# Kernel tuning notes

Hardware: AMD Instinct MI355X
Metric: run time of the kernel (lower is better)

Reference implementation:

```python
import jax, jax.numpy as jnp
import numpy as np

H = 128

def _gru_cell(x, h, w_ih, w_hh, b_ih, b_hh):
    # PyTorch GRUCell semantics; w_* are [3H, H], gate order r, z, n.
    gi = x @ w_ih.T + b_ih
    gh = h @ w_hh.T + b_hh
    ir, iz, in_ = jnp.split(gi, 3, axis=-1)
    hr, hz, hn = jnp.split(gh, 3, axis=-1)
    r = jax.nn.sigmoid(ir + hr)
    z = jax.nn.sigmoid(iz + hz)
    n = jnp.tanh(in_ + r * hn)
    return (1.0 - z) * n + z * h


def setup_inputs() -> dict:
    key = jax.random.key(0)
    ks = jax.random.split(key, 24)
    s = 0.05
    d = {}
    d["weapon_features"] = jax.random.normal(ks[0], (4, 8, 64, 4), jnp.float32)
    d["target_features"] = jax.random.normal(ks[1], (4, 8, 64, 4), jnp.float32)
    d["edge_features"] = jax.random.uniform(ks[2], (4, 8, 64, 64, 1), jnp.float32)
    # projections (torch Linear convention: weight [out, in])
    d["wp_w"] = jax.random.normal(ks[3], (H, 4), jnp.float32) * s
    d["wp_b"] = jnp.zeros((H,), jnp.float32)
    d["tp_w"] = jax.random.normal(ks[4], (H, 4), jnp.float32) * s
    d["tp_b"] = jnp.zeros((H,), jnp.float32)
    d["ep_w"] = jax.random.normal(ks[5], (H, 1), jnp.float32) * s
    d["ep_b"] = jnp.zeros((H,), jnp.float32)
    # message / edge-update linears [H, 3H]
    d["eu_w"] = jax.random.normal(ks[6], (H, 3 * H), jnp.float32) * s
    d["eu_b"] = jnp.zeros((H,), jnp.float32)
    d["wm_w"] = jax.random.normal(ks[7], (H, 3 * H), jnp.float32) * s
    d["wm_b"] = jnp.zeros((H,), jnp.float32)
    d["tm_w"] = jax.random.normal(ks[8], (H, 3 * H), jnp.float32) * s
    d["tm_b"] = jnp.zeros((H,), jnp.float32)
    # GRU cells
    d["gru_w_ih_w"] = jax.random.normal(ks[9], (3 * H, H), jnp.float32) * s
    d["gru_w_hh_w"] = jax.random.normal(ks[10], (3 * H, H), jnp.float32) * s
    d["gru_b_ih_w"] = jnp.zeros((3 * H,), jnp.float32)
    d["gru_b_hh_w"] = jnp.zeros((3 * H,), jnp.float32)
    d["gru_w_ih_t"] = jax.random.normal(ks[11], (3 * H, H), jnp.float32) * s
    d["gru_w_hh_t"] = jax.random.normal(ks[12], (3 * H, H), jnp.float32) * s
    d["gru_b_ih_t"] = jnp.zeros((3 * H,), jnp.float32)
    d["gru_b_hh_t"] = jnp.zeros((3 * H,), jnp.float32)
    return d


def reference(weapon_features, target_features, edge_features,
              wp_w, wp_b, tp_w, tp_b, ep_w, ep_b,
              eu_w, eu_b, wm_w, wm_b, tm_w, tm_b,
              gru_w_ih_w, gru_w_hh_w, gru_b_ih_w, gru_b_hh_w,
              gru_w_ih_t, gru_w_hh_t, gru_b_ih_t, gru_b_hh_t):
    B, P, W = weapon_features.shape[:3]
    T = target_features.shape[2]
    h = wp_w.shape[0]

    weapon_h = weapon_features @ wp_w.T + wp_b          # [B,P,W,H]
    target_h = target_features @ tp_w.T + tp_b          # [B,P,T,H]
    edge_h = edge_features @ ep_w.T + ep_b              # [B,P,W,T,H]

    # edge_update(cat([w_exp, t_exp, edge_h])) == sum of three slice-linears,
    # broadcast-added; avoids materializing the [B,P,W,T,3H] concat.
    ea, eb, ec = eu_w[:, :h], eu_w[:, h:2 * h], eu_w[:, 2 * h:]
    edge_pre = ((weapon_h @ ea.T)[:, :, :, None, :]
                + (target_h @ eb.T)[:, :, None, :, :]
                + edge_h @ ec.T + eu_b)
    edge_h_new = jnp.tanh(edge_pre)                     # [B,P,W,T,H]

    # weapon_msg(cat([w_exp, t_exp, edge_h_new])).sum(dim=3)
    wa, wb, wc = wm_w[:, :h], wm_w[:, h:2 * h], wm_w[:, 2 * h:]
    weapon_msgs = (T * (weapon_h @ wa.T)
                   + (target_h.sum(axis=2) @ wb.T)[:, :, None, :]
                   + edge_h_new.sum(axis=3) @ wc.T
                   + T * wm_b)                          # [B,P,W,H]

    # target_msg(cat([t_exp, w_exp, edge_h_new])).sum(dim=2)
    ta, tb, tc = tm_w[:, :h], tm_w[:, h:2 * h], tm_w[:, 2 * h:]
    target_msgs = (W * (target_h @ ta.T)
                   + (weapon_h.sum(axis=2) @ tb.T)[:, :, None, :]
                   + edge_h_new.sum(axis=2) @ tc.T
                   + W * tm_b)                          # [B,P,T,H]

    weapon_h_new = _gru_cell(weapon_msgs.reshape(-1, h), weapon_h.reshape(-1, h),
                             gru_w_ih_w, gru_w_hh_w, gru_b_ih_w, gru_b_hh_w)
    weapon_h_new = weapon_h_new.reshape(B, P, W, h)

    target_h_new = _gru_cell(target_msgs.reshape(-1, h), target_h.reshape(-1, h),
                             gru_w_ih_t, gru_w_hh_t, gru_b_ih_t, gru_b_hh_t)
    target_h_new = target_h_new.reshape(B, P, T, h)

    return weapon_h_new, target_h_new, edge_h_new
```

## Files before the change

### kernel.cpp

```cpp
#include <hip/hip_runtime.h>

#define DEV __device__ __forceinline__

constexpr int H  = 128;
constexpr int BP = 32;
constexpr int NR = 2048;

constexpr int WH_OFF    = 0;
constexpr int TH_OFF    = WH_OFF + NR*H;
constexpr int WHS_OFF   = TH_OFF + NR*H;
constexpr int THS_OFF   = WHS_OFF + BP*H;
constexpr int V1_OFF    = THS_OFF + BP*H;
constexpr int C0_OFF    = V1_OFF + H;
constexpr int WT1_OFF   = C0_OFF + H;
constexpr int WT2_OFF   = WT1_OFF + 128*640;
constexpr int WCT_OFF   = WT2_OFF + 128*640;
constexpr int TCT_OFF   = WCT_OFF + 128*128;
constexpr int WIHWT_OFF = TCT_OFF + 128*128;
constexpr int WIHTT_OFF = WIHWT_OFF + 128*384;
constexpr int WBT_OFF   = WIHTT_OFF + 128*384;
constexpr int TBT_OFF   = WBT_OFF + 128*128;
constexpr int OUT1_OFF  = TBT_OFF + 128*128;
constexpr int OUT2_OFF  = OUT1_OFF + NR*640;
constexpr int ESW_OFF   = OUT2_OFF + NR*640;
constexpr int ESTP_OFF  = ESW_OFF + NR*H;
constexpr int MSGW_OFF  = ESTP_OFF + 16*NR*H;
constexpr int MSGT_OFF  = MSGW_OFF + NR*H;
constexpr int GIW_OFF   = MSGT_OFF + NR*H;
constexpr int GIT_OFF   = GIW_OFF + NR*384;
constexpr int WBV_OFF   = GIT_OFF + NR*384;
constexpr int TBV_OFF   = WBV_OFF + BP*H;

DEV float fast_tanh(float x) {
  float e = __builtin_amdgcn_exp2f(x * 2.8853900817779268f);
  return fmaf(-2.0f, __builtin_amdgcn_rcpf(e + 1.0f), 1.0f);
}
DEV float fast_sigmoid(float x) {
  float e = __builtin_amdgcn_exp2f(x * -1.4426950408889634f);
  return __builtin_amdgcn_rcpf(1.0f + e);
}

__global__ __launch_bounds__(256) void k0_transpose(
    const float* __restrict__ eu_w, const float* __restrict__ wm_w,
    const float* __restrict__ tm_w,
    const float* __restrict__ whh_w, const float* __restrict__ whh_t,
    const float* __restrict__ wih_w, const float* __restrict__ wih_t,
    float* __restrict__ ws)
{
  __shared__ float T[128*133];
  int tt = blockIdx.x, tid = threadIdx.x;
  const float* src; int rs = 384, co = 0, row0 = 0, dsto, ldd, j0;
  switch (tt) {
    case 0:  src=eu_w;  dsto=WT1_OFF; ldd=640; j0=0;   break;
    case 1:  src=wm_w;  dsto=WT1_OFF; ldd=640; j0=128; break;
    case 2: case 3: case 4:
      src=whh_w; rs=128; row0=(tt-2)*128; dsto=WT1_OFF; ldd=640; j0=256+(tt-2)*128; break;
    case 5:  src=eu_w;  co=128; dsto=WT2_OFF; ldd=640; j0=0; break;
    case 6:  src=tm_w;  dsto=WT2_OFF; ldd=640; j0=128; break;
    case 7: case 8: case 9:
      src=whh_t; rs=128; row0=(tt-7)*128; dsto=WT2_OFF; ldd=640; j0=256+(tt-7)*128; break;
    case 10: src=wm_w; co=256; dsto=WCT_OFF; ldd=128; j0=0; break;
    case 11: src=tm_w; co=256; dsto=TCT_OFF; ldd=128; j0=0; break;
    case 12: src=wm_w; co=128; dsto=WBT_OFF; ldd=128; j0=0; break;
    case 13: src=tm_w; co=128; dsto=TBT_OFF; ldd=128; j0=0; break;
    case 14: case 15: case 16:
      src=wih_w; rs=128; row0=(tt-14)*128; dsto=WIHWT_OFF; ldd=384; j0=(tt-14)*128; break;
    default:
      src=wih_t; rs=128; row0=(tt-17)*128; dsto=WIHTT_OFF; ldd=384; j0=(tt-17)*128; break;
  }
  #pragma unroll
  for (int q = 0; q < 16; ++q) {
    int idx = q*1024 + tid*4;
    int r = idx >> 7, c = idx & 127;
    float4 v = *(const float4*)&src[(row0 + r)*rs + co + c];
    float* t = &T[r*133 + c];
    t[0]=v.x; t[1]=v.y; t[2]=v.z; t[3]=v.w;
  }
  __syncthreads();
  float* dst = ws + dsto;
  #pragma unroll
  for (int q = 0; q < 64; ++q) {
    int idx = q*256 + tid;
    int k = idx >> 7, j = idx & 127;
    dst[k*ldd + j0 + j] = T[j*133 + k];
  }
}

__global__ __launch_bounds__(256) void k1_proj(
    const float* __restrict__ wf, const float* __restrict__ tf,
    const float* __restrict__ wp_w, const float* __restrict__ wp_b,
    const float* __restrict__ tp_w, const float* __restrict__ tp_b,
    const float* __restrict__ eu_w,
    const float* __restrict__ ep_w, const float* __restrict__ ep_b,
    const float* __restrict__ eu_b,
    float* __restrict__ ws)
{
  __shared__ float fs[2][32][4];
  int bid = blockIdx.x, tid = threadIdx.x;
  if (bid < 2048) {
    int gid = bid*256 + tid;
    int m = gid >> 7;
    int j = gid & 127;
    int side = m >> 11;
    int n = m & 2047;
    const float* F  = side ? tf : wf;
    const float* Pw = side ? tp_w : wp_w;
    const float* Pb = side ? tp_b : wp_b;
    float4 x  = *(const float4*)&F[n*4];
    float4 wv = *(const float4*)&Pw[j*4];
    float v = x.x*wv.x + x.y*wv.y + x.z*wv.z + x.w*wv.w + Pb[j];
    ws[(side ? TH_OFF : WH_OFF) + n*H + j] = v;
  } else {
    {
      int side = tid >> 7, r = tid & 127;
      int bp = r >> 2, c = r & 3;
      const float* F = side ? tf : wf;
      float s = 0.f;
      #pragma unroll 8
      for (int w = 0; w < 64; ++w) s += F[bp*256 + w*4 + c];
      fs[side][bp][c] = s;
    }
    __syncthreads();
    {
      int side = tid >> 7, j = tid & 127;
      const float* Pw = side ? tp_w : wp_w;
      const float* Pb = side ? tp_b : wp_b;
      float4 wv = *(const float4*)&Pw[j*4];
      float pb = Pb[j] * 64.f;
      float* dst = ws + (side ? THS_OFF : WHS_OFF) + j;
      #pragma unroll 4
      for (int bp = 0; bp < 32; ++bp) {
        float4 f = *(const float4*)&fs[side][bp][0];
        dst[bp*128] = f.x*wv.x + f.y*wv.y + f.z*wv.z + f.w*wv.w + pb;
      }
    }
    if (tid < 128) {
      int j = tid;
      float s1 = 0.f, s0 = 0.f;
      for (int k = 0; k < 128; ++k) {
        float ec = eu_w[j*384 + 256 + k];
        s1 = fmaf(ec, ep_w[k], s1);
        s0 = fmaf(ec, ep_b[k], s0);
      }
      ws[V1_OFF + j] = s1;
      ws[C0_OFF + j] = s0 + eu_b[j];
    }
  }
}

#define FMA4(A, s, Wv) do { A.x = fmaf(s, Wv.x, A.x); A.y = fmaf(s, Wv.y, A.y); \
                            A.z = fmaf(s, Wv.z, A.z); A.w = fmaf(s, Wv.w, A.w); } while (0)

DEV void stage_x_direct(float* Xs, const float* __restrict__ X, int row0, int tid) {
  const float* src = X + row0*128;
  #pragma unroll
  for (int q = 0; q < 4; ++q) {
    int idx = q*1024 + tid*4;
    *(float4*)&Xs[idx] = *(const float4*)&src[idx];
  }
}

DEV void stage_x_sum16(float* Xs, const float* __restrict__ base, int row0, int tid) {
  #pragma unroll
  for (int q = 0; q < 4; ++q) {
    int idx = q*1024 + tid*4;
    float4 s = *(const float4*)&base[row0*128 + idx];
    #pragma unroll
    for (int wt = 1; wt < 16; ++wt) {
      float4 v = *(const float4*)&base[wt*(NR*H) + row0*128 + idx];
      s.x += v.x; s.y += v.y; s.z += v.z; s.w += v.w;
    }
    *(float4*)&Xs[idx] = s;
  }
}

DEV void gemm_core(const float* __restrict__ Wt, int ldw, int j0,
                   const float* Xs, float* Ws, int tid, float4 acc[4])
{
  const int tc = tid & 31, tr = tid >> 5;
  const int jj = tc*4, r0 = tr*4;
  #pragma unroll
  for (int i = 0; i < 4; ++i) acc[i] = make_float4(0.f, 0.f, 0.f, 0.f);
  for (int kc = 0; kc < 128; kc += 32) {
    __syncthreads();
    #pragma unroll
    for (int q = 0; q < 4; ++q) {
      int idx = q*1024 + tid*4;
      int kk = idx >> 7, j = idx & 127;
      *(float4*)&Ws[idx] = *(const float4*)&Wt[(kc+kk)*ldw + j0 + j];
    }
    __syncthreads();
    #pragma unroll
    for (int kk = 0; kk < 32; kk += 4) {
      float4 w0 = *(const float4*)&Ws[(kk+0)*128 + jj];
      float4 w1 = *(const float4*)&Ws[(kk+1)*128 + jj];
      float4 w2 = *(const float4*)&Ws[(kk+2)*128 + jj];
      float4 w3 = *(const float4*)&Ws[(kk+3)*128 + jj];
      #pragma unroll
      for (int rr = 0; rr < 4; ++rr) {
        float4 xq = *(const float4*)&Xs[(r0+rr)*128 + kc + kk];
        FMA4(acc[rr], xq.x, w0);
        FMA4(acc[rr], xq.y, w1);
        FMA4(acc[rr], xq.z, w2);
        FMA4(acc[rr], xq.w, w3);
      }
    }
  }
}

__global__ __launch_bounds__(256) void k3_gemm1(float* __restrict__ ws)
{
  __shared__ float Xs[32*128];
  __shared__ float Wsh[32*128];
  int bid = blockIdx.x, tid = threadIdx.x;
  const int tc = tid & 31, tr = tid >> 5;
  const int jj = tc*4, r0 = tr*4;
  float4 acc[4];
  if (bid < 640) {
    int side = bid >= 320;
    int b2 = bid - (side ? 320 : 0);
    int rt = b2 & 63, ct = b2 >> 6;
    int row0 = rt*32;
    stage_x_direct(Xs, ws + (side ? TH_OFF : WH_OFF), row0, tid);
    gemm_core(ws + (side ? WT2_OFF : WT1_OFF), 640, ct*128, Xs, Wsh, tid, acc);
    float* C = ws + (side ? OUT2_OFF : OUT1_OFF);
    #pragma unroll
    for (int rr = 0; rr < 4; ++rr)
      *(float4*)&C[(row0+r0+rr)*640 + ct*128 + jj] = acc[rr];
  } else {
    int which = bid - 640;
    stage_x_direct(Xs, ws + (which ? WHS_OFF : THS_OFF), 0, tid);
    gemm_core(ws + (which ? TBT_OFF : WBT_OFF), 128, 0, Xs, Wsh, tid, acc);
    float* C = ws + (which ? TBV_OFF : WBV_OFF);
    #pragma unroll
    for (int rr = 0; rr < 4; ++rr)
      *(float4*)&C[(r0+rr)*128 + jj] = acc[rr];
  }
}

__global__ __launch_bounds__(256) void k4_edge(
    const float* __restrict__ ef, float* __restrict__ ws, float* __restrict__ out)
{
  __shared__ float Bs[64*128];
  __shared__ float e_lds[4*64];
  __shared__ float red[2][4][128];
  int bid = blockIdx.x, tid = threadIdx.x;
  int bp = bid >> 4, wq = bid & 15;
  int j = tid & 127, tsel = tid >> 7;
  float v1j = ws[V1_OFF + j], c0j = ws[C0_OFF + j];
  {
    const float* o2 = ws + OUT2_OFF + bp*64*640;
    #pragma unroll
    for (int q = 0; q < 8; ++q) {
      int idx = q*256 + tid;
      int t = idx >> 5, jq = (idx & 31)*4;
      *(float4*)&Bs[t*128 + jq] = *(const float4*)&o2[t*640 + jq];
    }
  }
  if (tid < 64) {
    int w = tid >> 4, t4 = (tid & 15)*4;
    *(float4*)&e_lds[w*64 + t4] = *(const float4*)&ef[bp*4096 + (wq*4 + w)*64 + t4];
  }
  float a_reg[4];
  #pragma unroll
  for (int w = 0; w < 4; ++w)
    a_reg[w] = ws[OUT1_OFF + (bp*64 + wq*4 + w)*640 + j];
  __syncthreads();
  float tsum[4] = {0.f, 0.f, 0.f, 0.f};
  float* edst = out + 524288 + (bp*64 + wq*4)*8192 + j;
  float* pdst = ws + ESTP_OFF + wq*(NR*H) + bp*64*128 + j;
  for (int i = 0; i < 32; ++i) {
    int t = 2*i + tsel;
    float base = Bs[t*128 + j] + c0j;
    float wsum = 0.f;
    #pragma unroll
    for (int w = 0; w < 4; ++w) {
      float ev = e_lds[w*64 + t];
      float pre = a_reg[w] + fmaf(ev, v1j, base);
      float hv = fast_tanh(pre);
      __builtin_nontemporal_store(hv, &edst[w*8192 + t*128]);
      tsum[w] += hv;
      wsum += hv;
    }
    pdst[t*128] = wsum;
  }
  #pragma unroll
  for (int w = 0; w < 4; ++w) red[tsel][w][j] = tsum[w];
  __syncthreads();
  if (tsel == 0) {
    #pragma unroll
    for (int w = 0; w < 4; ++w)
      ws[ESW_OFF + (bp*64 + wq*4 + w)*128 + j] = red[0][w][j] + red[1][w][j];
  }
}

__global__ __launch_bounds__(256) void k5_gemm2(
    float* __restrict__ ws, const float* __restrict__ wm_b, const float* __restrict__ tm_b)
{
  __shared__ float Xs[32*128];
  __shared__ float Wsh[32*128];
  int bid = blockIdx.x, tid = threadIdx.x;
  int side = bid >> 6, rt = bid & 63;
  int row0 = rt*32;
  const int tc = tid & 31, tr = tid >> 5;
  const int jj = tc*4, r0 = tr*4;
  if (side == 0) stage_x_direct(Xs, ws + ESW_OFF, row0, tid);
  else           stage_x_sum16(Xs, ws + ESTP_OFF, row0, tid);
  float4 acc[4];
  gemm_core(ws + (side ? TCT_OFF : WCT_OFF), 128, 0, Xs, Wsh, tid, acc);
  const float* OUTx = ws + (side ? OUT2_OFF : OUT1_OFF);
  const float* BV   = ws + (side ? TBV_OFF : WBV_OFF);
  const float* mb   = side ? tm_b : wm_b;
  float* MSG        = ws + (side ? MSGT_OFF : MSGW_OFF);
  float4 b4 = *(const float4*)&mb[jj];
  #pragma unroll
  for (int rr = 0; rr < 4; ++rr) {
    int n = row0 + r0 + rr;
    float4 wa4 = *(const float4*)&OUTx[n*640 + 128 + jj];
    float4 bv4 = *(const float4*)&BV[(n >> 6)*128 + jj];
    float4 r;
    r.x = acc[rr].x + 64.f*(wa4.x + b4.x) + bv4.x;
    r.y = acc[rr].y + 64.f*(wa4.y + b4.y) + bv4.y;
    r.z = acc[rr].z + 64.f*(wa4.z + b4.z) + bv4.z;
    r.w = acc[rr].w + 64.f*(wa4.w + b4.w) + bv4.w;
    *(float4*)&MSG[n*128 + jj] = r;
  }
}

__global__ __launch_bounds__(256) void k6_gemm3(float* __restrict__ ws)
{
  __shared__ float Xs[32*128];
  __shared__ float Wsh[32*128];
  int bid = blockIdx.x, tid = threadIdx.x;
  int side = bid >= 192;
  int b2 = bid - (side ? 192 : 0);
  int rt = b2 & 63, ct = b2 >> 6;
  int row0 = rt*32;
  const int tc = tid & 31, tr = tid >> 5;
  const int jj = tc*4, r0 = tr*4;
  stage_x_direct(Xs, ws + (side ? MSGT_OFF : MSGW_OFF), row0, tid);
  float4 acc[4];
  gemm_core(ws + (side ? WIHTT_OFF : WIHWT_OFF), 384, ct*128, Xs, Wsh, tid, acc);
  float* C = ws + (side ? GIT_OFF : GIW_OFF);
  #pragma unroll
  for (int rr = 0; rr < 4; ++rr)
    *(float4*)&C[(row0+r0+rr)*384 + ct*128 + jj] = acc[rr];
}

__global__ __launch_bounds__(256) void k7_gru(
    const float* __restrict__ ws, float* __restrict__ out,
    const float* __restrict__ bih_w, const float* __restrict__ bhh_w,
    const float* __restrict__ bih_t, const float* __restrict__ bhh_t)
{
  int gid = blockIdx.x*256 + threadIdx.x;
  int m = gid >> 7, j = gid & 127;
  int side = m >> 11, n = m & 2047;
  const float* GI = ws + (side ? GIT_OFF : GIW_OFF) + n*384;
  const float* GH = ws + (side ? OUT2_OFF : OUT1_OFF) + n*640 + 256;
  const float* Hv = ws + (side ? TH_OFF : WH_OFF) + n*128;
  const float* bi = side ? bih_t : bih_w;
  const float* bh = side ? bhh_t : bhh_w;
  float gir = GI[j]       + bi[j];
  float giz = GI[128 + j] + bi[128 + j];
  float gin = GI[256 + j] + bi[256 + j];
  float ghr = GH[j]       + bh[j];
  float ghz = GH[128 + j] + bh[128 + j];
  float ghn = GH[256 + j] + bh[256 + j];
  float r  = fast_sigmoid(gir + ghr);
  float z  = fast_sigmoid(giz + ghz);
  float nn = fast_tanh(gin + r*ghn);
  float h  = Hv[j];
  out[side*262144 + n*128 + j] = (1.f - z)*nn + z*h;
}

extern "C" void kernel_launch(void* const* d_in, const int* in_sizes, int n_in,
                              void* d_out, int out_size, void* d_ws, size_t ws_size,
                              hipStream_t stream)
{
  const float* wf    = (const float*)d_in[0];
  const float* tf    = (const float*)d_in[1];
  const float* ef    = (const float*)d_in[2];
  const float* wp_w  = (const float*)d_in[3];
  const float* wp_b  = (const float*)d_in[4];
  const float* tp_w  = (const float*)d_in[5];
  const float* tp_b  = (const float*)d_in[6];
  const float* ep_w  = (const float*)d_in[7];
  const float* ep_b  = (const float*)d_in[8];
  const float* eu_w  = (const float*)d_in[9];
  const float* eu_b  = (const float*)d_in[10];
  const float* wm_w  = (const float*)d_in[11];
  const float* wm_b  = (const float*)d_in[12];
  const float* tm_w  = (const float*)d_in[13];
  const float* tm_b  = (const float*)d_in[14];
  const float* wih_w = (const float*)d_in[15];
  const float* whh_w = (const float*)d_in[16];
  const float* bih_w = (const float*)d_in[17];
  const float* bhh_w = (const float*)d_in[18];
  const float* wih_t = (const float*)d_in[19];
  const float* whh_t = (const float*)d_in[20];
  const float* bih_t = (const float*)d_in[21];
  const float* bhh_t = (const float*)d_in[22];
  float* ws  = (float*)d_ws;
  float* out = (float*)d_out;

  hipLaunchKernelGGL(k0_transpose, dim3(20), dim3(256), 0, stream,
                     eu_w, wm_w, tm_w, whh_w, whh_t, wih_w, wih_t, ws);
  hipLaunchKernelGGL(k1_proj, dim3(2049), dim3(256), 0, stream,
                     wf, tf, wp_w, wp_b, tp_w, tp_b, eu_w, ep_w, ep_b, eu_b, ws);
  hipLaunchKernelGGL(k3_gemm1, dim3(642),  dim3(256), 0, stream, ws);
  hipLaunchKernelGGL(k4_edge,  dim3(512),  dim3(256), 0, stream, ef, ws, out);
  hipLaunchKernelGGL(k5_gemm2, dim3(128),  dim3(256), 0, stream, ws, wm_b, tm_b);
  hipLaunchKernelGGL(k6_gemm3, dim3(384),  dim3(256), 0, stream, ws);
  hipLaunchKernelGGL(k7_gru,   dim3(2048), dim3(256), 0, stream, ws, out,
                     bih_w, bhh_w, bih_t, bhh_t);
}
```

Before: 189.2 us.

## Merge transpose into projection kernel, enlarge gemm1 tiles, widen edge and GRU work

The weight-transpose kernel becomes extra blocks of the projection kernel, removing one launch. gemm1 moves to 64-row tiles with 8 accumulators per thread to improve weight reuse. The edge kernel now handles 8 weapons per block, which halves the partial target-sum buffers that gemm2 must reduce. The GRU kernel uses float4 loads and nontemporal stores. Each change trades fewer blocks and launches for more registers and LDS per block, which can lower occupancy.

```diff
diff --git a/kernel.cpp b/kernel.cpp
--- a/kernel.cpp
+++ b/kernel.cpp
@@ -24,7 +24,7 @@
 constexpr int OUT2_OFF  = OUT1_OFF + NR*640;
 constexpr int ESW_OFF   = OUT2_OFF + NR*640;
 constexpr int ESTP_OFF  = ESW_OFF + NR*H;
-constexpr int MSGW_OFF  = ESTP_OFF + 16*NR*H;
+constexpr int MSGW_OFF  = ESTP_OFF + 8*NR*H;
 constexpr int MSGT_OFF  = MSGW_OFF + NR*H;
 constexpr int GIW_OFF   = MSGT_OFF + NR*H;
 constexpr int GIT_OFF   = GIW_OFF + NR*384;
@@ -40,62 +40,18 @@
   return __builtin_amdgcn_rcpf(1.0f + e);
 }
 
-__global__ __launch_bounds__(256) void k0_transpose(
+__global__ __launch_bounds__(256) void ka_prep(
+    const float* __restrict__ wf, const float* __restrict__ tf,
+    const float* __restrict__ wp_w, const float* __restrict__ wp_b,
+    const float* __restrict__ tp_w, const float* __restrict__ tp_b,
     const float* __restrict__ eu_w, const float* __restrict__ wm_w,
     const float* __restrict__ tm_w,
     const float* __restrict__ whh_w, const float* __restrict__ whh_t,
     const float* __restrict__ wih_w, const float* __restrict__ wih_t,
-    float* __restrict__ ws)
-{
-  __shared__ float T[128*133];
-  int tt = blockIdx.x, tid = threadIdx.x;
-  const float* src; int rs = 384, co = 0, row0 = 0, dsto, ldd, j0;
-  switch (tt) {
-    case 0:  src=eu_w;  dsto=WT1_OFF; ldd=640; j0=0;   break;
-    case 1:  src=wm_w;  dsto=WT1_OFF; ldd=640; j0=128; break;
-    case 2: case 3: case 4:
-      src=whh_w; rs=128; row0=(tt-2)*128; dsto=WT1_OFF; ldd=640; j0=256+(tt-2)*128; break;
-    case 5:  src=eu_w;  co=128; dsto=WT2_OFF; ldd=640; j0=0; break;
-    case 6:  src=tm_w;  dsto=WT2_OFF; ldd=640; j0=128; break;
-    case 7: case 8: case 9:
-      src=whh_t; rs=128; row0=(tt-7)*128; dsto=WT2_OFF; ldd=640; j0=256+(tt-7)*128; break;
-    case 10: src=wm_w; co=256; dsto=WCT_OFF; ldd=128; j0=0; break;
-    case 11: src=tm_w; co=256; dsto=TCT_OFF; ldd=128; j0=0; break;
-    case 12: src=wm_w; co=128; dsto=WBT_OFF; ldd=128; j0=0; break;
-    case 13: src=tm_w; co=128; dsto=TBT_OFF; ldd=128; j0=0; break;
-    case 14: case 15: case 16:
-      src=wih_w; rs=128; row0=(tt-14)*128; dsto=WIHWT_OFF; ldd=384; j0=(tt-14)*128; break;
-    default:
-      src=wih_t; rs=128; row0=(tt-17)*128; dsto=WIHTT_OFF; ldd=384; j0=(tt-17)*128; break;
-  }
-  #pragma unroll
-  for (int q = 0; q < 16; ++q) {
-    int idx = q*1024 + tid*4;
-    int r = idx >> 7, c = idx & 127;
-    float4 v = *(const float4*)&src[(row0 + r)*rs + co + c];
-    float* t = &T[r*133 + c];
-    t[0]=v.x; t[1]=v.y; t[2]=v.z; t[3]=v.w;
-  }
-  __syncthreads();
-  float* dst = ws + dsto;
-  #pragma unroll
-  for (int q = 0; q < 64; ++q) {
-    int idx = q*256 + tid;
-    int k = idx >> 7, j = idx & 127;
-    dst[k*ldd + j0 + j] = T[j*133 + k];
-  }
-}
-
-__global__ __launch_bounds__(256) void k1_proj(
-    const float* __restrict__ wf, const float* __restrict__ tf,
-    const float* __restrict__ wp_w, const float* __restrict__ wp_b,
-    const float* __restrict__ tp_w, const float* __restrict__ tp_b,
-    const float* __restrict__ eu_w,
     const float* __restrict__ ep_w, const float* __restrict__ ep_b,
     const float* __restrict__ eu_b,
     float* __restrict__ ws)
 {
-  __shared__ float fs[2][32][4];
   int bid = blockIdx.x, tid = threadIdx.x;
   if (bid < 2048) {
     int gid = bid*256 + tid;
@@ -110,7 +66,8 @@
     float4 wv = *(const float4*)&Pw[j*4];
     float v = x.x*wv.x + x.y*wv.y + x.z*wv.z + x.w*wv.w + Pb[j];
     ws[(side ? TH_OFF : WH_OFF) + n*H + j] = v;
-  } else {
+  } else if (bid == 2048) {
+    __shared__ float fs[2][32][4];
     {
       int side = tid >> 7, r = tid & 127;
       int bp = r >> 2, c = r & 3;
@@ -145,13 +102,51 @@
       ws[V1_OFF + j] = s1;
       ws[C0_OFF + j] = s0 + eu_b[j];
     }
+  } else {
+    __shared__ float T[128*133];
+    int tt = bid - 2049;
+    const float* src; int rs = 384, co = 0, row0 = 0, dsto, ldd, j0;
+    switch (tt) {
+      case 0:  src=eu_w;  dsto=WT1_OFF; ldd=640; j0=0;   break;
+      case 1:  src=wm_w;  dsto=WT1_OFF; ldd=640; j0=128; break;
+      case 2: case 3: case 4:
+        src=whh_w; rs=128; row0=(tt-2)*128; dsto=WT1_OFF; ldd=640; j0=256+(tt-2)*128; break;
+      case 5:  src=eu_w;  co=128; dsto=WT2_OFF; ldd=640; j0=0; break;
+      case 6:  src=tm_w;  dsto=WT2_OFF; ldd=640; j0=128; break;
+      case 7: case 8: case 9:
+        src=whh_t; rs=128; row0=(tt-7)*128; dsto=WT2_OFF; ldd=640; j0=256+(tt-7)*128; break;
+      case 10: src=wm_w; co=256; dsto=WCT_OFF; ldd=128; j0=0; break;
+      case 11: src=tm_w; co=256; dsto=TCT_OFF; ldd=128; j0=0; break;
+      case 12: src=wm_w; co=128; dsto=WBT_OFF; ldd=128; j0=0; break;
+      case 13: src=tm_w; co=128; dsto=TBT_OFF; ldd=128; j0=0; break;
+      case 14: case 15: case 16:
+        src=wih_w; rs=128; row0=(tt-14)*128; dsto=WIHWT_OFF; ldd=384; j0=(tt-14)*128; break;
+      default:
+        src=wih_t; rs=128; row0=(tt-17)*128; dsto=WIHTT_OFF; ldd=384; j0=(tt-17)*128; break;
+    }
+    #pragma unroll
+    for (int q = 0; q < 16; ++q) {
+      int idx = q*1024 + tid*4;
+      int r = idx >> 7, c = idx & 127;
+      float4 v = *(const float4*)&src[(row0 + r)*rs + co + c];
+      float* t = &T[r*133 + c];
+      t[0]=v.x; t[1]=v.y; t[2]=v.z; t[3]=v.w;
+    }
+    __syncthreads();
+    float* dst = ws + dsto;
+    #pragma unroll
+    for (int q = 0; q < 64; ++q) {
+      int idx = q*256 + tid;
+      int k = idx >> 7, j = idx & 127;
+      dst[k*ldd + j0 + j] = T[j*133 + k];
+    }
   }
 }
 
 #define FMA4(A, s, Wv) do { A.x = fmaf(s, Wv.x, A.x); A.y = fmaf(s, Wv.y, A.y); \
                             A.z = fmaf(s, Wv.z, A.z); A.w = fmaf(s, Wv.w, A.w); } while (0)
 
-DEV void stage_x_direct(float* Xs, const float* __restrict__ X, int row0, int tid) {
+DEV void stage_x32(float* Xs, const float* __restrict__ X, int row0, int tid) {
   const float* src = X + row0*128;
   #pragma unroll
   for (int q = 0; q < 4; ++q) {
@@ -160,13 +155,22 @@
   }
 }
 
-DEV void stage_x_sum16(float* Xs, const float* __restrict__ base, int row0, int tid) {
+DEV void stage_x64(float* Xs, const float* __restrict__ X, int row0, int tid) {
+  const float* src = X + row0*128;
+  #pragma unroll
+  for (int q = 0; q < 8; ++q) {
+    int idx = q*1024 + tid*4;
+    *(float4*)&Xs[idx] = *(const float4*)&src[idx];
+  }
+}
+
+DEV void stage_x_sum8(float* Xs, const float* __restrict__ base, int row0, int tid) {
   #pragma unroll
   for (int q = 0; q < 4; ++q) {
     int idx = q*1024 + tid*4;
     float4 s = *(const float4*)&base[row0*128 + idx];
     #pragma unroll
-    for (int wt = 1; wt < 16; ++wt) {
+    for (int wt = 1; wt < 8; ++wt) {
       float4 v = *(const float4*)&base[wt*(NR*H) + row0*128 + idx];
       s.x += v.x; s.y += v.y; s.z += v.z; s.w += v.w;
     }
@@ -174,8 +178,8 @@
   }
 }
 
-DEV void gemm_core(const float* __restrict__ Wt, int ldw, int j0,
-                   const float* Xs, float* Ws, int tid, float4 acc[4])
+DEV void gemm_core32(const float* __restrict__ Wt, int ldw, int j0,
+                     const float* Xs, float* Ws, int tid, float4 acc[4])
 {
   const int tc = tid & 31, tr = tid >> 5;
   const int jj = tc*4, r0 = tr*4;
@@ -208,44 +212,81 @@
   }
 }
 
-__global__ __launch_bounds__(256) void k3_gemm1(float* __restrict__ ws)
-{
-  __shared__ float Xs[32*128];
+DEV void gemm_core64(const float* __restrict__ Wt, int ldw, int j0,
+                     const float* Xs, float* Ws, int tid, float4 acc[8])
+{
+  const int tc = tid & 31, tr = tid >> 5;
+  const int jj = tc*4, r0 = tr*8;
+  #pragma unroll
+  for (int i = 0; i < 8; ++i) acc[i] = make_float4(0.f, 0.f, 0.f, 0.f);
+  for (int kc = 0; kc < 128; kc += 32) {
+    __syncthreads();
+    #pragma unroll
+    for (int q = 0; q < 4; ++q) {
+      int idx = q*1024 + tid*4;
+      int kk = idx >> 7, j = idx & 127;
+      *(float4*)&Ws[idx] = *(const float4*)&Wt[(kc+kk)*ldw + j0 + j];
+    }
+    __syncthreads();
+    #pragma unroll
+    for (int kk = 0; kk < 32; kk += 4) {
+      float4 w0 = *(const float4*)&Ws[(kk+0)*128 + jj];
+      float4 w1 = *(const float4*)&Ws[(kk+1)*128 + jj];
+      float4 w2 = *(const float4*)&Ws[(kk+2)*128 + jj];
+      float4 w3 = *(const float4*)&Ws[(kk+3)*128 + jj];
+      #pragma unroll
+      for (int rr = 0; rr < 8; ++rr) {
+        float4 xq = *(const float4*)&Xs[(r0+rr)*128 + kc + kk];
+        FMA4(acc[rr], xq.x, w0);
+        FMA4(acc[rr], xq.y, w1);
+        FMA4(acc[rr], xq.z, w2);
+        FMA4(acc[rr], xq.w, w3);
+      }
+    }
+  }
+}
+
+__global__ __launch_bounds__(256) void kb_gemm1(float* __restrict__ ws)
+{
+  __shared__ float Xs[64*128];
   __shared__ float Wsh[32*128];
   int bid = blockIdx.x, tid = threadIdx.x;
   const int tc = tid & 31, tr = tid >> 5;
-  const int jj = tc*4, r0 = tr*4;
-  float4 acc[4];
-  if (bid < 640) {
-    int side = bid >= 320;
-    int b2 = bid - (side ? 320 : 0);
-    int rt = b2 & 63, ct = b2 >> 6;
-    int row0 = rt*32;
-    stage_x_direct(Xs, ws + (side ? TH_OFF : WH_OFF), row0, tid);
-    gemm_core(ws + (side ? WT2_OFF : WT1_OFF), 640, ct*128, Xs, Wsh, tid, acc);
+  const int jj = tc*4;
+  if (bid < 320) {
+    int side = bid >= 160;
+    int b2 = bid - (side ? 160 : 0);
+    int rt = b2 & 31, ct = b2 >> 5;
+    int row0 = rt*64;
+    stage_x64(Xs, ws + (side ? TH_OFF : WH_OFF), row0, tid);
+    float4 acc[8];
+    gemm_core64(ws + (side ? WT2_OFF : WT1_OFF), 640, ct*128, Xs, Wsh, tid, acc);
     float* C = ws + (side ? OUT2_OFF : OUT1_OFF);
-    #pragma unroll
-    for (int rr = 0; rr < 4; ++rr)
+    const int r0 = tr*8;
+    #pragma unroll
+    for (int rr = 0; rr < 8; ++rr)
       *(float4*)&C[(row0+r0+rr)*640 + ct*128 + jj] = acc[rr];
   } else {
-    int which = bid - 640;
-    stage_x_direct(Xs, ws + (which ? WHS_OFF : THS_OFF), 0, tid);
-    gemm_core(ws + (which ? TBT_OFF : WBT_OFF), 128, 0, Xs, Wsh, tid, acc);
+    int which = bid - 320;
+    stage_x32(Xs, ws + (which ? WHS_OFF : THS_OFF), 0, tid);
+    float4 acc[4];
+    gemm_core32(ws + (which ? TBT_OFF : WBT_OFF), 128, 0, Xs, Wsh, tid, acc);
     float* C = ws + (which ? TBV_OFF : WBV_OFF);
+    const int r0 = tr*4;
     #pragma unroll
     for (int rr = 0; rr < 4; ++rr)
       *(float4*)&C[(r0+rr)*128 + jj] = acc[rr];
   }
 }
 
-__global__ __launch_bounds__(256) void k4_edge(
+__global__ __launch_bounds__(256) void kc_edge(
     const float* __restrict__ ef, float* __restrict__ ws, float* __restrict__ out)
 {
   __shared__ float Bs[64*128];
-  __shared__ float e_lds[4*64];
-  __shared__ float red[2][4][128];
+  __shared__ float e_lds[8*64];
+  __shared__ float red[2][8][128];
   int bid = blockIdx.x, tid = threadIdx.x;
-  int bp = bid >> 4, wq = bid & 15;
+  int bp = bid >> 3, wq = bid & 7;
   int j = tid & 127, tsel = tid >> 7;
   float v1j = ws[V1_OFF + j], c0j = ws[C0_OFF + j];
   {
@@ -257,24 +298,24 @@
       *(float4*)&Bs[t*128 + jq] = *(const float4*)&o2[t*640 + jq];
     }
   }
-  if (tid < 64) {
+  if (tid < 128) {
     int w = tid >> 4, t4 = (tid & 15)*4;
-    *(float4*)&e_lds[w*64 + t4] = *(const float4*)&ef[bp*4096 + (wq*4 + w)*64 + t4];
-  }
-  float a_reg[4];
-  #pragma unroll
-  for (int w = 0; w < 4; ++w)
-    a_reg[w] = ws[OUT1_OFF + (bp*64 + wq*4 + w)*640 + j];
+    *(float4*)&e_lds[w*64 + t4] = *(const float4*)&ef[bp*4096 + (wq*8 + w)*64 + t4];
+  }
+  float a_reg[8];
+  #pragma unroll
+  for (int w = 0; w < 8; ++w)
+    a_reg[w] = ws[OUT1_OFF + (bp*64 + wq*8 + w)*640 + j];
   __syncthreads();
-  float tsum[4] = {0.f, 0.f, 0.f, 0.f};
-  float* edst = out + 524288 + (bp*64 + wq*4)*8192 + j;
+  float tsum[8] = {0,0,0,0,0,0,0,0};
+  float* edst = out + 524288 + (bp*64 + wq*8)*8192 + j;
   float* pdst = ws + ESTP_OFF + wq*(NR*H) + bp*64*128 + j;
   for (int i = 0; i < 32; ++i) {
     int t = 2*i + tsel;
     float base = Bs[t*128 + j] + c0j;
     float wsum = 0.f;
     #pragma unroll
-    for (int w = 0; w < 4; ++w) {
+    for (int w = 0; w < 8; ++w) {
       float ev = e_lds[w*64 + t];
       float pre = a_reg[w] + fmaf(ev, v1j, base);
       float hv = fast_tanh(pre);
@@ -285,16 +326,16 @@
     pdst[t*128] = wsum;
   }
   #pragma unroll
-  for (int w = 0; w < 4; ++w) red[tsel][w][j] = tsum[w];
+  for (int w = 0; w < 8; ++w) red[tsel][w][j] = tsum[w];
   __syncthreads();
   if (tsel == 0) {
     #pragma unroll
-    for (int w = 0; w < 4; ++w)
-      ws[ESW_OFF + (bp*64 + wq*4 + w)*128 + j] = red[0][w][j] + red[1][w][j];
-  }
-}
-
-__global__ __launch_bounds__(256) void k5_gemm2(
+    for (int w = 0; w < 8; ++w)
+      ws[ESW_OFF + (bp*64 + wq*8 + w)*128 + j] = red[0][w][j] + red[1][w][j];
+  }
+}
+
+__global__ __launch_bounds__(256) void kd_gemm2(
     float* __restrict__ ws, const float* __restrict__ wm_b, const float* __restrict__ tm_b)
 {
   __shared__ float Xs[32*128];
@@ -304,10 +345,10 @@
   int row0 = rt*32;
   const int tc = tid & 31, tr = tid >> 5;
   const int jj = tc*4, r0 = tr*4;
-  if (side == 0) stage_x_direct(Xs, ws + ESW_OFF, row0, tid);
-  else           stage_x_sum16(Xs, ws + ESTP_OFF, row0, tid);
+  if (side == 0) stage_x32(Xs, ws + ESW_OFF, row0, tid);
+  else           stage_x_sum8(Xs, ws + ESTP_OFF, row0, tid);
   float4 acc[4];
-  gemm_core(ws + (side ? TCT_OFF : WCT_OFF), 128, 0, Xs, Wsh, tid, acc);
+  gemm_core32(ws + (side ? TCT_OFF : WCT_OFF), 128, 0, Xs, Wsh, tid, acc);
   const float* OUTx = ws + (side ? OUT2_OFF : OUT1_OFF);
   const float* BV   = ws + (side ? TBV_OFF : WBV_OFF);
   const float* mb   = side ? tm_b : wm_b;
@@ -327,7 +368,7 @@
   }
 }
 
-__global__ __launch_bounds__(256) void k6_gemm3(float* __restrict__ ws)
+__global__ __launch_bounds__(256) void ke_gemm3(float* __restrict__ ws)
 {
   __shared__ float Xs[32*128];
   __shared__ float Wsh[32*128];
@@ -338,39 +379,54 @@
   int row0 = rt*32;
   const int tc = tid & 31, tr = tid >> 5;
   const int jj = tc*4, r0 = tr*4;
-  stage_x_direct(Xs, ws + (side ? MSGT_OFF : MSGW_OFF), row0, tid);
+  stage_x32(Xs, ws + (side ? MSGT_OFF : MSGW_OFF), row0, tid);
   float4 acc[4];
-  gemm_core(ws + (side ? WIHTT_OFF : WIHWT_OFF), 384, ct*128, Xs, Wsh, tid, acc);
+  gemm_core32(ws + (side ? WIHTT_OFF : WIHWT_OFF), 384, ct*128, Xs, Wsh, tid, acc);
   float* C = ws + (side ? GIT_OFF : GIW_OFF);
   #pragma unroll
   for (int rr = 0; rr < 4; ++rr)
     *(float4*)&C[(row0+r0+rr)*384 + ct*128 + jj] = acc[rr];
 }
 
-__global__ __launch_bounds__(256) void k7_gru(
+__global__ __launch_bounds__(256) void kf_gru(
     const float* __restrict__ ws, float* __restrict__ out,
     const float* __restrict__ bih_w, const float* __restrict__ bhh_w,
     const float* __restrict__ bih_t, const float* __restrict__ bhh_t)
 {
   int gid = blockIdx.x*256 + threadIdx.x;
-  int m = gid >> 7, j = gid & 127;
-  int side = m >> 11, n = m & 2047;
+  int jj = (gid & 31)*4;
+  int n  = (gid >> 5) & 2047;
+  int side = gid >> 16;
   const float* GI = ws + (side ? GIT_OFF : GIW_OFF) + n*384;
   const float* GH = ws + (side ? OUT2_OFF : OUT1_OFF) + n*640 + 256;
   const float* Hv = ws + (side ? TH_OFF : WH_OFF) + n*128;
   const float* bi = side ? bih_t : bih_w;
   const float* bh = side ? bhh_t : bhh_w;
-  float gir = GI[j]       + bi[j];
-  float giz = GI[128 + j] + bi[128 + j];
-  float gin = GI[256 + j] + bi[256 + j];
-  float ghr = GH[j]       + bh[j];
-  float ghz = GH[128 + j] + bh[128 + j];
-  float ghn = GH[256 + j] + bh[256 + j];
-  float r  = fast_sigmoid(gir + ghr);
-  float z  = fast_sigmoid(giz + ghz);
-  float nn = fast_tanh(gin + r*ghn);
-  float h  = Hv[j];
-  out[side*262144 + n*128 + j] = (1.f - z)*nn + z*h;
+  float4 gir = *(const float4*)&GI[jj];
+  float4 giz = *(const float4*)&GI[128 + jj];
+  float4 gin = *(const float4*)&GI[256 + jj];
+  float4 ghr = *(const float4*)&GH[jj];
+  float4 ghz = *(const float4*)&GH[128 + jj];
+  float4 ghn = *(const float4*)&GH[256 + jj];
+  float4 bir = *(const float4*)&bi[jj];
+  float4 biz = *(const float4*)&bi[128 + jj];
+  float4 bin = *(const float4*)&bi[256 + jj];
+  float4 bhr = *(const float4*)&bh[jj];
+  float4 bhz = *(const float4*)&bh[128 + jj];
+  float4 bhn = *(const float4*)&bh[256 + jj];
+  float4 h4  = *(const float4*)&Hv[jj];
+  float4 o;
+  #define GRU1(c) do { \
+    float r = fast_sigmoid(gir.c + bir.c + ghr.c + bhr.c); \
+    float z = fast_sigmoid(giz.c + biz.c + ghz.c + bhz.c); \
+    float nn = fast_tanh(gin.c + bin.c + r*(ghn.c + bhn.c)); \
+    o.c = (1.f - z)*nn + z*h4.c; } while (0)
+  GRU1(x); GRU1(y); GRU1(z); GRU1(w);
+  #undef GRU1
+  __builtin_nontemporal_store(o.x, &out[side*262144 + n*128 + jj + 0]);
+  __builtin_nontemporal_store(o.y, &out[side*262144 + n*128 + jj + 1]);
+  __builtin_nontemporal_store(o.z, &out[side*262144 + n*128 + jj + 2]);
+  __builtin_nontemporal_store(o.w, &out[side*262144 + n*128 + jj + 3]);
 }
 
 extern "C" void kernel_launch(void* const* d_in, const int* in_sizes, int n_in,
@@ -403,14 +459,13 @@
   float* ws  = (float*)d_ws;
   float* out = (float*)d_out;
 
-  hipLaunchKernelGGL(k0_transpose, dim3(20), dim3(256), 0, stream,
-                     eu_w, wm_w, tm_w, whh_w, whh_t, wih_w, wih_t, ws);
-  hipLaunchKernelGGL(k1_proj, dim3(2049), dim3(256), 0, stream,
-                     wf, tf, wp_w, wp_b, tp_w, tp_b, eu_w, ep_w, ep_b, eu_b, ws);
-  hipLaunchKernelGGL(k3_gemm1, dim3(642),  dim3(256), 0, stream, ws);
-  hipLaunchKernelGGL(k4_edge,  dim3(512),  dim3(256), 0, stream, ef, ws, out);
-  hipLaunchKernelGGL(k5_gemm2, dim3(128),  dim3(256), 0, stream, ws, wm_b, tm_b);
-  hipLaunchKernelGGL(k6_gemm3, dim3(384),  dim3(256), 0, stream, ws);
-  hipLaunchKernelGGL(k7_gru,   dim3(2048), dim3(256), 0, stream, ws, out,
+  hipLaunchKernelGGL(ka_prep, dim3(2069), dim3(256), 0, stream,
+                     wf, tf, wp_w, wp_b, tp_w, tp_b, eu_w, wm_w, tm_w,
+                     whh_w, whh_t, wih_w, wih_t, ep_w, ep_b, eu_b, ws);
+  hipLaunchKernelGGL(kb_gemm1, dim3(322),  dim3(256), 0, stream, ws);
+  hipLaunchKernelGGL(kc_edge,  dim3(256),  dim3(256), 0, stream, ef, ws, out);
+  hipLaunchKernelGGL(kd_gemm2, dim3(128),  dim3(256), 0, stream, ws, wm_b, tm_b);
+  hipLaunchKernelGGL(ke_gemm3, dim3(384),  dim3(256), 0, stream, ws);
+  hipLaunchKernelGGL(kf_gru,   dim3(512),  dim3(256), 0, stream, ws, out,
                      bih_w, bhh_w, bih_t, bhh_t);
 }
```

Measured after the change: 186.6 us. Within noise of the previous version (-1.4%).
